# Kernel optimization log

Measured on AMD Instinct MI355X. Metric: run time of the kernel, lower is better.

## Reference

```python
import jax, jax.numpy as jnp
import numpy as np

B, N, E, H = 2, 2048, 2048, 16
D = E // H  # head_dim = 128


def setup_inputs() -> dict:
    key = jax.random.key(0)
    k1, k2, k3, k4 = jax.random.split(key, 4)
    x = jax.random.normal(k1, (B, N, E), dtype=jnp.float32)
    Wq = jax.random.normal(k2, (E, E), dtype=jnp.float32) * 0.02
    Wkv = jax.random.normal(k3, (2 * E, E), dtype=jnp.float32) * 0.02
    Wout = jax.random.normal(k4, (E, E), dtype=jnp.float32) * 0.02
    return {"x": x, "Wq": Wq, "Wkv": Wkv, "Wout": Wout}


def reference(x, Wq, Wkv, Wout):
    # projections (torch Linear: y = x @ W.T)
    q = x @ Wq.T                      # [b, n, e]
    kv = x @ Wkv.T                    # [b, n, 2e]
    k, v = jnp.split(kv, 2, axis=-1)  # each [b, n, e]

    def split_heads(t):
        return t.reshape(B, N, H, D).transpose(0, 2, 1, 3)  # [b, h, n, d]

    q, k, v = split_heads(q), split_heads(k), split_heads(v)

    scale = D ** -0.5
    sim = jnp.einsum('bhid,bhjd->bhij', q * scale, k)  # [b, h, n, n]

    # causal mask: triu(j - i + 1) masks strictly-future positions
    mask_value = -jnp.finfo(sim.dtype).max
    causal_mask = jnp.triu(jnp.ones((N, N), dtype=bool), k=1)
    sim = jnp.where(causal_mask, mask_value, sim)

    attn = jax.nn.softmax(sim, axis=-1)
    out = jnp.einsum('bhij,bhjd->bhid', attn, v)  # [b, h, n, d]
    out = out.transpose(0, 2, 1, 3).reshape(B, N, E)
    return out @ Wout.T
```

## Files before the change

### kernel.cpp

```cpp
#include <hip/hip_runtime.h>


typedef __bf16 bf16;
typedef bf16 bf16x2 __attribute__((ext_vector_type(2)));
typedef bf16 bf16x4 __attribute__((ext_vector_type(4)));
typedef bf16 bf16x8 __attribute__((ext_vector_type(8)));
typedef float f32x4 __attribute__((ext_vector_type(4)));
typedef float f32x16 __attribute__((ext_vector_type(16)));

typedef const __attribute__((address_space(1))) void cg_void;
typedef __attribute__((address_space(3))) void lds_void;

#define MFMA16(a, b, c) __builtin_amdgcn_mfma_f32_16x16x32_bf16((a), (b), (c), 0, 0, 0)
#define MFMA32(a, b, c) __builtin_amdgcn_mfma_f32_32x32x16_bf16((a), (b), (c), 0, 0, 0)

__device__ __forceinline__ void async_load16(const bf16* g, bf16* l) {
  __builtin_amdgcn_global_load_lds((cg_void*)g, (lds_void*)l, 16, 0, 0);
}

__global__ __launch_bounds__(256) void cast_all_kernel(
    const float* __restrict__ x, const float* __restrict__ wq,
    const float* __restrict__ wkv, const float* __restrict__ wout,
    bf16* __restrict__ xb, bf16* __restrict__ wqkvb, bf16* __restrict__ woutb) {
  long i = (long)blockIdx.x * 256 + threadIdx.x;
  const float* src; bf16* dst; long off;
  if (i < 1048576)      { src = x;    dst = xb;            off = i; }
  else if (i < 2621440) { src = wq;   dst = wqkvb;         off = i - 1048576;
                          if (off >= 524288) { src = wkv; dst = wqkvb + 4194304; off -= 524288; } }
  else                  { src = wout; dst = woutb;         off = i - 2621440; }
  float4 f0 = ((const float4*)src)[2 * off];
  float4 f1 = ((const float4*)src)[2 * off + 1];
  bf16x8 o;
  o[0] = (bf16)f0.x; o[1] = (bf16)f0.y; o[2] = (bf16)f0.z; o[3] = (bf16)f0.w;
  o[4] = (bf16)f1.x; o[5] = (bf16)f1.y; o[6] = (bf16)f1.z; o[7] = (bf16)f1.w;
  ((bf16x8*)dst)[off] = o;
}

template <typename OutT>
__global__ __launch_bounds__(256, 4)
void gemm_bt_kernel(const bf16* __restrict__ A, const bf16* __restrict__ B,
                    OutT* __restrict__ C, int K, int NN) {
  __shared__ __attribute__((aligned(16))) bf16 As[128 * 32];
  __shared__ __attribute__((aligned(16))) bf16 Bs[128 * 32];
  const int tid = threadIdx.x;
  const int wave = tid >> 6, lane = tid & 63;
  const int quad = lane >> 4, l15 = lane & 15;
  const int m0 = blockIdx.y * 128, n0 = blockIdx.x * 128;
  const int wm = (wave >> 1) * 64, wn = (wave & 1) * 64;

  f32x4 acc[4][4];
#pragma unroll
  for (int i = 0; i < 4; ++i)
#pragma unroll
    for (int j = 0; j < 4; ++j) acc[i][j] = {0.f, 0.f, 0.f, 0.f};

  const int srow = tid >> 2;
  const int scol = (tid & 3) * 8;
  const bf16* aG = A + (size_t)(m0 + srow) * K + scol;
  const bf16* bG = B + (size_t)(n0 + srow) * K + scol;
  bf16* aL = As + srow * 32 + scol;
  bf16* bL = Bs + srow * 32 + scol;
  const size_t gstep = (size_t)64 * K;

  for (int kt = 0; kt < K; kt += 32) {
    __syncthreads();
    async_load16(aG, aL);
    async_load16(aG + gstep, aL + 64 * 32);
    async_load16(bG, bL);
    async_load16(bG + gstep, bL + 64 * 32);
    aG += 32; bG += 32;
    __syncthreads();

    bf16x8 af[4], bfr[4];
#pragma unroll
    for (int i = 0; i < 4; ++i)
      af[i] = *(const bf16x8*)(As + (wm + i * 16 + l15) * 32 + quad * 8);
#pragma unroll
    for (int j = 0; j < 4; ++j)
      bfr[j] = *(const bf16x8*)(Bs + (wn + j * 16 + l15) * 32 + quad * 8);
#pragma unroll
    for (int i = 0; i < 4; ++i)
#pragma unroll
      for (int j = 0; j < 4; ++j) acc[i][j] = MFMA16(af[i], bfr[j], acc[i][j]);
  }

#pragma unroll
  for (int i = 0; i < 4; ++i) {
#pragma unroll
    for (int r = 0; r < 4; ++r) {
      int row = m0 + wm + i * 16 + quad * 4 + r;
      size_t base = (size_t)row * NN + n0 + wn + l15;
#pragma unroll
      for (int j = 0; j < 4; ++j) C[base + j * 16] = (OutT)acc[i][j][r];
    }
  }
}

__global__ __launch_bounds__(256) void vtrans_kernel(const bf16* __restrict__ qkvb,
                                                     bf16* __restrict__ vt) {
  constexpr int QKV = 6144, NSEQ = 2048, E = 2048;
  __shared__ __attribute__((aligned(16))) bf16 Ts[64 * 64];
  const int t = threadIdx.x;
  const int n0 = blockIdx.x * 64, f0 = blockIdx.y * 64, bb = blockIdx.z;
#pragma unroll
  for (int p = 0; p < 2; ++p) {
    int c = p * 256 + t;
    int i = c >> 3, jc = c & 7;
    bf16x8 v = *(const bf16x8*)(qkvb + (size_t)(bb * NSEQ + n0 + i) * QKV + 4096 + f0 + jc * 8);
    *(bf16x8*)(Ts + i * 64 + ((jc + i) & 7) * 8) = v;
  }
  __syncthreads();
#pragma unroll
  for (int p = 0; p < 2; ++p) {
    int c = p * 256 + t;
    int fl = c >> 3, nl = (c & 7) * 8;
    bf16x8 o;
#pragma unroll
    for (int k = 0; k < 8; ++k) {
      int row = nl + k;
      o[k] = Ts[row * 64 + (((fl >> 3) + row) & 7) * 8 + (fl & 7)];
    }
    *(bf16x8*)(vt + (size_t)(bb * E + f0 + fl) * NSEQ + n0 + nl) = o;
  }
}

__global__ __launch_bounds__(256, 2)
void attn_kernel(const bf16* __restrict__ qkv, const bf16* __restrict__ vt,
                 bf16* __restrict__ yb) {
  constexpr int NSEQ = 2048, E = 2048, QKV = 6144;
  __shared__ __attribute__((aligned(16))) bf16 Ks[64 * 128];
  __shared__ __attribute__((aligned(16))) bf16 Vs[128 * 64];
  const int tid = threadIdx.x;
  const int wave = tid >> 6, lane = tid & 63;
  const int l31 = lane & 31, half = lane >> 5;
  const int b = blockIdx.x >> 4, h = blockIdx.x & 15;
  const int slot = blockIdx.y;
  const int qt = (slot < 8) ? slot : 23 - slot;
  const float c1 = 0.08838834764831845f * 1.44269504088896f;

  const int qrow = qt * 128 + wave * 32 + l31;
  bf16x8 qf[8];
  {
    const bf16* qp = qkv + (size_t)(b * NSEQ + qrow) * QKV + h * 128 + half * 8;
#pragma unroll
    for (int k8 = 0; k8 < 8; ++k8) qf[k8] = *(const bf16x8*)(qp + k8 * 16);
  }

  float m = -3.0e38f, l = 0.f;
  f32x16 accO[4];
#pragma unroll
  for (int md = 0; md < 4; ++md)
#pragma unroll
    for (int r = 0; r < 16; ++r) accO[md][r] = 0.f;

  const int krow_s = tid >> 4, kch_s = tid & 15;
  const int vrow_s = tid >> 3, vch_s = tid & 7;
  bf16* kdst = Ks + tid * 8;
  bf16* vdst = Vs + tid * 8;

  const int diag = 2 * qt + (wave >> 1);
  const int ktmax = 2 * qt + 1;

  union PU { unsigned u; bf16x2 h; };
  union FU { bf16x8 v; unsigned u[4]; };

  for (int kt = 0; kt <= ktmax; ++kt) {
    __syncthreads();
#pragma unroll
    for (int p = 0; p < 4; ++p) {
      int r = p * 16 + krow_s;
      int gch = kch_s ^ (r & 7);
      const bf16* gsrc = qkv + (size_t)(b * NSEQ + kt * 64 + r) * QKV + 2048 + h * 128 + gch * 8;
      async_load16(gsrc, kdst + p * 2048);
    }
#pragma unroll
    for (int p = 0; p < 4; ++p) {
      int r = p * 32 + vrow_s;
      int gch = vch_s ^ (r & 7);
      const bf16* gsrc = vt + ((size_t)b * E + h * 128 + r) * NSEQ + kt * 64 + gch * 8;
      async_load16(gsrc, vdst + p * 2048);
    }
    __syncthreads();

    if (kt > diag) continue;

    f32x16 st[2];
#pragma unroll
    for (int mt = 0; mt < 2; ++mt)
#pragma unroll
      for (int r = 0; r < 16; ++r) st[mt][r] = 0.f;
#pragma unroll
    for (int k8 = 0; k8 < 8; ++k8) {
#pragma unroll
      for (int mt = 0; mt < 2; ++mt) {
        int row = mt * 32 + l31;
        int sl = (k8 * 2 + half) ^ (row & 7);
        bf16x8 kf = *(const bf16x8*)(Ks + row * 128 + sl * 8);
        st[mt] = MFMA32(kf, qf[k8], st[mt]);
      }
    }

    if (kt == diag) {
#pragma unroll
      for (int mt = 0; mt < 2; ++mt)
#pragma unroll
        for (int r = 0; r < 16; ++r) {
          int t = kt * 64 + mt * 32 + (r & 3) + 8 * (r >> 2) + 4 * half;
          if (t > qrow) st[mt][r] = -3.0e38f;
        }
    }

    float mx = -3.0e38f;
#pragma unroll
    for (int mt = 0; mt < 2; ++mt)
#pragma unroll
      for (int r = 0; r < 16; ++r) mx = fmaxf(mx, st[mt][r]);
    mx = fmaxf(mx, __shfl_xor(mx, 32));
    float mnew = fmaxf(m, mx);
    float alpha = exp2f((m - mnew) * c1);
    float mc = mnew * c1;
    m = mnew;

    float psum = 0.f;
    unsigned pown[2][4][2];
#pragma unroll
    for (int mt = 0; mt < 2; ++mt)
#pragma unroll
      for (int qd = 0; qd < 4; ++qd)
#pragma unroll
        for (int pr = 0; pr < 2; ++pr) {
          float p0 = exp2f(st[mt][qd * 4 + pr * 2] * c1 - mc);
          float p1 = exp2f(st[mt][qd * 4 + pr * 2 + 1] * c1 - mc);
          psum += p0 + p1;
          PU a; a.h[0] = (bf16)p0; a.h[1] = (bf16)p1;
          pown[mt][qd][pr] = a.u;
        }
    psum += __shfl_xor(psum, 32);
    l = l * alpha + psum;

#pragma unroll
    for (int md = 0; md < 4; ++md)
#pragma unroll
      for (int r = 0; r < 16; ++r) accO[md][r] *= alpha;

#pragma unroll
    for (int mt = 0; mt < 2; ++mt)
#pragma unroll
      for (int c = 0; c < 2; ++c) {
        const int qa = 2 * c, qb = 2 * c + 1;
        unsigned ra0 = __shfl_xor(pown[mt][qa][0], 32);
        unsigned ra1 = __shfl_xor(pown[mt][qa][1], 32);
        unsigned rb0 = __shfl_xor(pown[mt][qb][0], 32);
        unsigned rb1 = __shfl_xor(pown[mt][qb][1], 32);
        FU f;
        f.u[0] = half ? rb0 : pown[mt][qa][0];
        f.u[1] = half ? rb1 : pown[mt][qa][1];
        f.u[2] = half ? pown[mt][qb][0] : ra0;
        f.u[3] = half ? pown[mt][qb][1] : ra1;
        const int kk = mt * 2 + c;
#pragma unroll
        for (int md = 0; md < 4; ++md) {
          int row = md * 32 + l31;
          bf16x8 vf = *(const bf16x8*)(Vs + row * 64 + (((kk * 2 + half) ^ (row & 7)) * 8));
          accO[md] = MFMA32(vf, f.v, accO[md]);
        }
      }
  }

  float invl = 1.0f / l;
  bf16* yp = yb + (size_t)(b * NSEQ + qrow) * E + h * 128;
#pragma unroll
  for (int md = 0; md < 4; ++md)
#pragma unroll
    for (int rq = 0; rq < 4; ++rq) {
      bf16x4 o;
#pragma unroll
      for (int i = 0; i < 4; ++i) o[i] = (bf16)(accO[md][rq * 4 + i] * invl);
      *(bf16x4*)(yp + md * 32 + rq * 8 + half * 4) = o;
    }
}

extern "C" void kernel_launch(void* const* d_in, const int* in_sizes, int n_in,
                              void* d_out, int out_size, void* d_ws, size_t ws_size,
                              hipStream_t stream) {
  const float* x    = (const float*)d_in[0];
  const float* Wq   = (const float*)d_in[1];
  const float* Wkv  = (const float*)d_in[2];
  const float* Wout = (const float*)d_in[3];
  float* out = (float*)d_out;

  constexpr size_t NX = (size_t)2 * 2048 * 2048;
  constexpr size_t NW = (size_t)2048 * 2048;

  bf16* xb     = (bf16*)d_ws;
  bf16* wqkvb  = xb + NX;
  bf16* woutb  = wqkvb + 3 * NW;
  bf16* qkv_b  = woutb + NW;
  bf16* y_b    = qkv_b + 3 * NX;
  bf16* vt_b   = xb;

  cast_all_kernel<<<12288, 256, 0, stream>>>(x, Wq, Wkv, Wout, xb, wqkvb, woutb);

  gemm_bt_kernel<bf16><<<dim3(48, 32), 256, 0, stream>>>(xb, wqkvb, qkv_b, 2048, 6144);
  vtrans_kernel<<<dim3(32, 32, 2), 256, 0, stream>>>(qkv_b, vt_b);
  attn_kernel<<<dim3(32, 16), 256, 0, stream>>>(qkv_b, vt_b, y_b);
  gemm_bt_kernel<float><<<dim3(16, 32), 256, 0, stream>>>(y_b, woutb, out, 2048, 2048);
}
```

Measured before the change: 384.0 us.

## Double-buffer K/V tiles in attention and remap block ids for locality

The attention kernel now keeps two LDS buffers each for K and V. It preloads the first tile, and on every iteration it issues async loads for the next tile before computing on the current one. This removes one barrier per iteration and overlaps global-to-LDS traffic with the MFMA work. The grid becomes one-dimensional, and the block index is decoded so that neighbouring blocks share (batch, head) groups, which aims to improve L2 reuse of K/V. The cost is double the LDS per block.

```diff
diff --git a/kernel.cpp b/kernel.cpp
--- a/kernel.cpp
+++ b/kernel.cpp
@@ -128,15 +128,40 @@
 void attn_kernel(const bf16* __restrict__ qkv, const bf16* __restrict__ vt,
                  bf16* __restrict__ yb) {
   constexpr int NSEQ = 2048, E = 2048, QKV = 6144;
-  __shared__ __attribute__((aligned(16))) bf16 Ks[64 * 128];
-  __shared__ __attribute__((aligned(16))) bf16 Vs[128 * 64];
+  __shared__ __attribute__((aligned(16))) bf16 Ks[2][64 * 128];
+  __shared__ __attribute__((aligned(16))) bf16 Vs[2][128 * 64];
   const int tid = threadIdx.x;
   const int wave = tid >> 6, lane = tid & 63;
   const int l31 = lane & 31, half = lane >> 5;
-  const int b = blockIdx.x >> 4, h = blockIdx.x & 15;
-  const int slot = blockIdx.y;
+  const int id = blockIdx.x;
+  const int slot = (id >> 3) & 15;
+  const int bh = (id & 7) | ((id >> 7) << 3);
+  const int b = bh >> 4, h = bh & 15;
   const int qt = (slot < 8) ? slot : 23 - slot;
   const float c1 = 0.08838834764831845f * 1.44269504088896f;
+
+  const int krow_s = tid >> 4, kch_s = tid & 15;
+  const int vrow_s = tid >> 3, vch_s = tid & 7;
+  const bf16* kg = qkv + (size_t)(b * NSEQ) * QKV + 2048 + h * 128;
+  const bf16* vg = vt + (size_t)b * E * NSEQ + (size_t)(h * 128) * NSEQ;
+
+  const int diag = 2 * qt + (wave >> 1);
+  const int ktmax = 2 * qt + 1;
+
+  {
+    bf16* kdst = Ks[0] + tid * 8;
+    bf16* vdst = Vs[0] + tid * 8;
+#pragma unroll
+    for (int p = 0; p < 4; ++p) {
+      int r = p * 16 + krow_s;
+      async_load16(kg + (size_t)r * QKV + (kch_s ^ (r & 7)) * 8, kdst + p * 2048);
+    }
+#pragma unroll
+    for (int p = 0; p < 4; ++p) {
+      int r = p * 32 + vrow_s;
+      async_load16(vg + (size_t)r * NSEQ + (vch_s ^ (r & 7)) * 8, vdst + p * 2048);
+    }
+  }
 
   const int qrow = qt * 128 + wave * 32 + l31;
   bf16x8 qf[8];
@@ -153,36 +178,33 @@
 #pragma unroll
     for (int r = 0; r < 16; ++r) accO[md][r] = 0.f;
 
-  const int krow_s = tid >> 4, kch_s = tid & 15;
-  const int vrow_s = tid >> 3, vch_s = tid & 7;
-  bf16* kdst = Ks + tid * 8;
-  bf16* vdst = Vs + tid * 8;
-
-  const int diag = 2 * qt + (wave >> 1);
-  const int ktmax = 2 * qt + 1;
-
   union PU { unsigned u; bf16x2 h; };
   union FU { bf16x8 v; unsigned u[4]; };
 
   for (int kt = 0; kt <= ktmax; ++kt) {
+    const int cur = kt & 1;
     __syncthreads();
-#pragma unroll
-    for (int p = 0; p < 4; ++p) {
-      int r = p * 16 + krow_s;
-      int gch = kch_s ^ (r & 7);
-      const bf16* gsrc = qkv + (size_t)(b * NSEQ + kt * 64 + r) * QKV + 2048 + h * 128 + gch * 8;
-      async_load16(gsrc, kdst + p * 2048);
-    }
-#pragma unroll
-    for (int p = 0; p < 4; ++p) {
-      int r = p * 32 + vrow_s;
-      int gch = vch_s ^ (r & 7);
-      const bf16* gsrc = vt + ((size_t)b * E + h * 128 + r) * NSEQ + kt * 64 + gch * 8;
-      async_load16(gsrc, vdst + p * 2048);
-    }
-    __syncthreads();
+
+    if (kt < ktmax) {
+      const int nxt = kt + 1;
+      bf16* kdst = Ks[1 - cur] + tid * 8;
+      bf16* vdst = Vs[1 - cur] + tid * 8;
+#pragma unroll
+      for (int p = 0; p < 4; ++p) {
+        int r = p * 16 + krow_s;
+        async_load16(kg + (size_t)(nxt * 64 + r) * QKV + (kch_s ^ (r & 7)) * 8, kdst + p * 2048);
+      }
+#pragma unroll
+      for (int p = 0; p < 4; ++p) {
+        int r = p * 32 + vrow_s;
+        async_load16(vg + (size_t)r * NSEQ + nxt * 64 + (vch_s ^ (r & 7)) * 8, vdst + p * 2048);
+      }
+    }
 
     if (kt > diag) continue;
+
+    const bf16* ks = Ks[cur];
+    const bf16* vs = Vs[cur];
 
     f32x16 st[2];
 #pragma unroll
@@ -195,7 +217,7 @@
       for (int mt = 0; mt < 2; ++mt) {
         int row = mt * 32 + l31;
         int sl = (k8 * 2 + half) ^ (row & 7);
-        bf16x8 kf = *(const bf16x8*)(Ks + row * 128 + sl * 8);
+        bf16x8 kf = *(const bf16x8*)(ks + row * 128 + sl * 8);
         st[mt] = MFMA32(kf, qf[k8], st[mt]);
       }
     }
@@ -261,7 +283,7 @@
 #pragma unroll
         for (int md = 0; md < 4; ++md) {
           int row = md * 32 + l31;
-          bf16x8 vf = *(const bf16x8*)(Vs + row * 64 + (((kk * 2 + half) ^ (row & 7)) * 8));
+          bf16x8 vf = *(const bf16x8*)(vs + row * 64 + (((kk * 2 + half) ^ (row & 7)) * 8));
           accO[md] = MFMA32(vf, f.v, accO[md]);
         }
       }
@@ -303,6 +325,6 @@
 
   gemm_bt_kernel<bf16><<<dim3(48, 32), 256, 0, stream>>>(xb, wqkvb, qkv_b, 2048, 6144);
   vtrans_kernel<<<dim3(32, 32, 2), 256, 0, stream>>>(qkv_b, vt_b);
-  attn_kernel<<<dim3(32, 16), 256, 0, stream>>>(qkv_b, vt_b, y_b);
+  attn_kernel<<<512, 256, 0, stream>>>(qkv_b, vt_b, y_b);
   gemm_bt_kernel<float><<<dim3(16, 32), 256, 0, stream>>>(y_b, woutb, out, 2048, 2048);
 }
```

New measurement: 396.8 us. +3.3%, slower.
